# Kernel tuning notes

Measured on AMD Instinct MI355X. Metric: run time of the kernel, lower is better.

## Reference

```python
import jax, jax.numpy as jnp
import numpy as np

GRID_SIZE = 8
POSITIVE_MARGIN = 1.0
NEGATIVE_MARGIN = 0.2
LAMBDA_D = 250.0
B, Hc, Wc, D = 4, 60, 60, 64


def warp_points(points, homographies):
    """points: [N,2] in (y,x); homographies: [B,3,3]. Returns [B,N,2] in (y,x)."""
    n = points.shape[0]
    xy1 = jnp.concatenate([points[:, ::-1], jnp.ones((n, 1), points.dtype)], axis=-1)  # (x,y,1)
    w = jnp.einsum('bij,nj->bni', homographies, xy1)  # [B,N,3]
    w = w[..., :2] / w[..., 2:3]
    return w[..., ::-1]  # back to (y,x)


def setup_inputs() -> dict:
    key = jax.random.key(0)
    k1, k2, k3 = jax.random.split(key, 3)
    descriptors = jax.random.normal(k1, (B, Hc, Wc, D), dtype=jnp.float32)
    warped_descriptors = jax.random.normal(k2, (B, Hc, Wc, D), dtype=jnp.float32)
    # near-identity homographies so warped cell centers remain close to the grid
    homographies = jnp.eye(3, dtype=jnp.float32)[None] + 0.001 * jax.random.normal(
        k3, (B, 3, 3), dtype=jnp.float32)
    valid_mask = jnp.ones((B, Hc * GRID_SIZE, Wc * GRID_SIZE), dtype=jnp.float32)
    return {"descriptors": descriptors, "warped_descriptors": warped_descriptors,
            "homographies": homographies, "valid_mask": valid_mask}


def reference(descriptors, warped_descriptors, homographies, valid_mask):
    b, hc, wc, d = descriptors.shape
    g = GRID_SIZE

    # cell-center coordinates (y, x) at full resolution
    yy, xx = jnp.meshgrid(jnp.arange(hc), jnp.arange(wc), indexing='ij')
    coord_cells = jnp.stack([yy, xx], axis=-1).astype(jnp.float32) * g + g // 2  # [Hc,Wc,2]

    warped_coord_cells = warp_points(coord_cells.reshape(-1, 2), homographies)  # [B,Hc*Wc,2]
    cc = coord_cells.reshape(1, 1, 1, hc, wc, 2)
    wcc = warped_coord_cells.reshape(b, hc, wc, 1, 1, 2)
    cell_distances = jnp.linalg.norm(cc - wcc, axis=-1)  # [B,Hc,Wc,Hc,Wc]
    s = (cell_distances <= g - 0.5).astype(descriptors.dtype)

    # broadcast dot-product score tensor [B,Hc,Wc,Hc,Wc]
    dot = jnp.einsum('bijd,bkld->bijkl', descriptors, warped_descriptors)

    positive_dist = jnp.maximum(0.0, POSITIVE_MARGIN - dot)
    negative_dist = jnp.maximum(0.0, dot - NEGATIVE_MARGIN)
    loss = LAMBDA_D * s * positive_dist + (1.0 - s) * negative_dist

    # space-to-depth + prod over the g*g block == per-cell AND of the valid mask
    vm = valid_mask.reshape(b, hc, g, wc, g)
    vm = jnp.prod(vm, axis=(2, 4))  # [B,Hc,Wc]
    vm = vm.reshape(b, 1, 1, hc, wc)

    normalization = jnp.sum(vm) * jnp.float32(hc * wc)
    return jnp.sum(vm * loss) / normalization
```

## Files before the change

kernel.cpp:

```cpp
#include <hip/hip_runtime.h>
#include <hip/hip_bf16.h>
#include <hip/hip_fp8.h>

#define HC 60
#define WCC 60
#define DD 64
#define NCELL (HC * WCC)
#define NBC (4 * NCELL)
#define IMG (HC * 8)
#define MPAD 3840
#define NT2 30
#define GEMM_BLOCKS (NT2 * NT2 * 4)
#define CHUNK (GEMM_BLOCKS / 8)

#define CVT_BLOCKS 480
#define VM_BLOCKS 57
#define WC_BLOCKS 60
#define PREP_BLOCKS (CVT_BLOCKS + VM_BLOCKS + WC_BLOCKS)

typedef float f32x4 __attribute__((ext_vector_type(4)));
typedef unsigned long long u64x2 __attribute__((ext_vector_type(2)));

__device__ inline unsigned char f2fp8(float f) {
    __hip_fp8_e4m3 h(f);
    return h.__x;
}

__device__ inline void gload_lds16(const void* g, void* l) {
    __builtin_amdgcn_global_load_lds(
        (const __attribute__((address_space(1))) unsigned int*)g,
        (__attribute__((address_space(3))) unsigned int*)l, 16, 0, 0);
}

__device__ inline int div60(int v) { return (v * 17477) >> 20; }


__global__ __launch_bounds__(256) void dl_prep_kernel(
    const float* __restrict__ desc, const float* __restrict__ wdesc,
    const float* __restrict__ homog, const float* __restrict__ mask,
    unsigned char* __restrict__ descb, unsigned char* __restrict__ wdescb,
    float* __restrict__ vm, float* __restrict__ vpart, float2* __restrict__ wcent)
{
    const int bid = blockIdx.x;
    const int tid = threadIdx.x;

    if (bid < CVT_BLOCKS) {
        int k = bid & 7;
        int q = bid >> 3;
        int b = k >> 1;
        int wp = (k & 1) * 60 + q;
        int row = wp * 32 + (tid >> 3);
        int c = tid & 7;
        unsigned long long pa = 0ull, pb = 0ull;
        if (row < NCELL) {
            size_t src = ((size_t)(b * NCELL + row)) * DD + c * 8;
            float4 a0 = *(const float4*)(desc + src);
            float4 a1 = *(const float4*)(desc + src + 4);
            float4 b0 = *(const float4*)(wdesc + src);
            float4 b1 = *(const float4*)(wdesc + src + 4);
            pa = (unsigned long long)f2fp8(a0.x)
               | ((unsigned long long)f2fp8(a0.y) << 8)
               | ((unsigned long long)f2fp8(a0.z) << 16)
               | ((unsigned long long)f2fp8(a0.w) << 24)
               | ((unsigned long long)f2fp8(a1.x) << 32)
               | ((unsigned long long)f2fp8(a1.y) << 40)
               | ((unsigned long long)f2fp8(a1.z) << 48)
               | ((unsigned long long)f2fp8(a1.w) << 56);
            pb = (unsigned long long)f2fp8(b0.x)
               | ((unsigned long long)f2fp8(b0.y) << 8)
               | ((unsigned long long)f2fp8(b0.z) << 16)
               | ((unsigned long long)f2fp8(b0.w) << 24)
               | ((unsigned long long)f2fp8(b1.x) << 32)
               | ((unsigned long long)f2fp8(b1.y) << 40)
               | ((unsigned long long)f2fp8(b1.z) << 48)
               | ((unsigned long long)f2fp8(b1.w) << 56);
        }
        int pos = ((c & 3) * 16 + (c >> 2) * 8) ^ ((row & 3) << 4);
        size_t dst = ((size_t)b * MPAD + row) * 64 + pos;
        *(unsigned long long*)(descb + dst) = pa;
        *(unsigned long long*)(wdescb + dst) = pb;
    } else if (bid < CVT_BLOCKS + VM_BLOCKS) {
        int vb = bid - CVT_BLOCKS;
        int cell = vb * 256 + tid;
        float v = 0.f;
        if (cell < NBC) {
            int b = cell / NCELL;
            int rem = cell % NCELL;
            int k = rem / WCC, l = rem % WCC;
            const float* p = mask + (size_t)b * IMG * IMG + (size_t)(k * 8) * IMG + l * 8;
            float prod = 1.f;
#pragma unroll
            for (int dy = 0; dy < 8; ++dy) {
                float4 a0 = *(const float4*)(p + (size_t)dy * IMG);
                float4 a1 = *(const float4*)(p + (size_t)dy * IMG + 4);
                prod *= a0.x * a0.y * a0.z * a0.w * a1.x * a1.y * a1.z * a1.w;
            }
            vm[cell] = prod;
            v = prod;
        }
#pragma unroll
        for (int off = 32; off > 0; off >>= 1) v += __shfl_xor(v, off);
        __shared__ float sp[4];
        if ((tid & 63) == 0) sp[tid >> 6] = v;
        __syncthreads();
        if (tid == 0) vpart[vb] = sp[0] + sp[1] + sp[2] + sp[3];
    } else {
        int t = (bid - CVT_BLOCKS - VM_BLOCKS) * 256 + tid;
        int b = t / MPAD;
        int r = t - b * MPAD;
        float2 o;
        if (r < NCELL) {
            int i = div60(r);
            int j = r - i * WCC;
            const float* H = homog + b * 9;
            float x = (float)(j * 8 + 4), y = (float)(i * 8 + 4);
            float X2 = H[6] * x + H[7] * y + H[8];
            o.x = (H[3] * x + H[4] * y + H[5]) / X2;
            o.y = (H[0] * x + H[1] * y + H[2]) / X2;
        } else {
            o.x = 1e9f; o.y = 1e9f;
        }
        wcent[t] = o;
    }
}

__global__ __launch_bounds__(256, 3) void dl_gemm_loss_kernel(
    const unsigned char* __restrict__ descb, const unsigned char* __restrict__ wdescb,
    const float* __restrict__ vm, const float2* __restrict__ wcent,
    float* __restrict__ gpart)
{
    __shared__ unsigned char sA[128 * 64];
    __shared__ unsigned char sB[128 * 64];
    __shared__ float2 swc[128];
    __shared__ float swave[4];

    const int orig = blockIdx.x;
    const int tile = (orig & 7) * CHUNK + (orig >> 3);
    const int b = tile / (NT2 * NT2);
    const int rr = tile - b * (NT2 * NT2);
    const int x = rr / NT2;
    const int y = rr - x * NT2;
    const int m0 = x * 128;
    const int n0 = y * 128;

    const int tid = threadIdx.x;
    const int lane = tid & 63;
    const int wv = tid >> 6;

    const unsigned char* gA = descb + ((size_t)b * MPAD + m0) * 64;
    const unsigned char* gB = wdescb + ((size_t)b * MPAD + n0) * 64;

#pragma unroll
    for (int t = 0; t < 2; ++t) {
        gload_lds16(gA + t * 4096 + tid * 16, sA + t * 4096 + tid * 16);
        gload_lds16(gB + t * 4096 + tid * 16, sB + t * 4096 + tid * 16);
    }
    if (tid < 128) swc[tid] = wcent[b * MPAD + m0 + tid];

    const int wr = wv >> 1, wcs = wv & 1;
    const int frow = lane & 15;
    const int kg16 = (lane >> 4) * 16;

    float cyv[4], cxv[4], vmv[4];
#pragma unroll
    for (int fj = 0; fj < 4; ++fj) {
        int col = n0 + wcs * 64 + fj * 16 + frow;
        int k = div60(col);
        int l = col - k * WCC;
        cyv[fj] = (float)(k * 8 + 4);
        cxv[fj] = (float)(l * 8 + 4);
        vmv[fj] = (col < NCELL) ? vm[b * NCELL + col] : 0.f;
    }
    float wyl = wcent[b * MPAD + m0 + wr * 64 + lane].x;
    float wlo = wyl, whi = wyl;
#pragma unroll
    for (int off = 32; off > 0; off >>= 1) {
        wlo = fminf(wlo, __shfl_xor(wlo, off));
        whi = fmaxf(whi, __shfl_xor(whi, off));
    }
    int c0 = n0 + wcs * 64;
    float cy0 = (float)(div60(c0) * 8 + 4) - 7.5f;
    float cy1 = (float)(div60(c0 + 63) * 8 + 4) + 7.5f;
    bool full = (whi >= cy0) && (wlo <= cy1);

    __syncthreads();

    u64x2 afr[4], bfr[4];
#pragma unroll
    for (int f = 0; f < 4; ++f) {
        int ra = wr * 64 + f * 16 + frow;
        afr[f] = *(const u64x2*)(sA + ra * 64 + (kg16 ^ ((ra & 3) << 4)));
        int rb = wcs * 64 + f * 16 + frow;
        bfr[f] = *(const u64x2*)(sB + rb * 64 + (kg16 ^ ((rb & 3) << 4)));
    }

    f32x4 acc[4][4];
#pragma unroll
    for (int i2 = 0; i2 < 4; ++i2)
#pragma unroll
        for (int j2 = 0; j2 < 4; ++j2)
            acc[i2][j2] = (f32x4)(0.f);

#pragma unroll
    for (int kk = 0; kk < 2; ++kk)
#pragma unroll
        for (int fi = 0; fi < 4; ++fi)
#pragma unroll
            for (int fj = 0; fj < 4; ++fj)
                acc[fi][fj] = __builtin_amdgcn_mfma_f32_16x16x32_fp8_fp8(
                    (long long)afr[fi][kk], (long long)bfr[fj][kk],
                    acc[fi][fj], 0, 0, 0);

    float partial = 0.f;
    if (full) {
#pragma unroll
        for (int fi = 0; fi < 4; ++fi) {
#pragma unroll
            for (int q = 0; q < 4; ++q) {
                float2 w2 = swc[wr * 64 + fi * 16 + (lane >> 4) * 4 + q];
#pragma unroll
                for (int fj = 0; fj < 4; ++fj) {
                    float dot = acc[fi][fj][q];
                    float ddy = cyv[fj] - w2.x;
                    float ddx = cxv[fj] - w2.y;
                    float d2 = ddy * ddy + ddx * ddx;
                    float pos = 250.f * fmaxf(1.f - dot, 0.f) + 0.2f;
                    float neg = fmaxf(dot, 0.2f);
                    partial += vmv[fj] * ((d2 <= 56.25f) ? pos : neg);
                }
            }
        }
    } else {
#pragma unroll
        for (int fj = 0; fj < 4; ++fj) {
            float cs = 0.f;
#pragma unroll
            for (int fi = 0; fi < 4; ++fi)
#pragma unroll
                for (int q = 0; q < 4; ++q)
                    cs += fmaxf(acc[fi][fj][q], 0.2f);
            partial = fmaf(vmv[fj], cs, partial);
        }
    }

#pragma unroll
    for (int off = 32; off > 0; off >>= 1) partial += __shfl_xor(partial, off);
    if (lane == 0) swave[wv] = partial;
    __syncthreads();
    if (tid == 0)
        gpart[orig] = swave[0] + swave[1] + swave[2] + swave[3];
}

__global__ __launch_bounds__(256) void dl_final_kernel(
    const float* __restrict__ vpart, const float* __restrict__ gpart,
    float* __restrict__ out)
{
    int tid = threadIdx.x;
    float ls = 0.f, vs = 0.f;
    for (int i = tid; i < GEMM_BLOCKS; i += 256) ls += gpart[i];
    for (int i = tid; i < VM_BLOCKS; i += 256) vs += vpart[i];
#pragma unroll
    for (int off = 32; off > 0; off >>= 1) {
        ls += __shfl_xor(ls, off);
        vs += __shfl_xor(vs, off);
    }
    __shared__ float sl[4], sv[4];
    if ((tid & 63) == 0) { sl[tid >> 6] = ls; sv[tid >> 6] = vs; }
    __syncthreads();
    if (tid == 0) {
        float L = sl[0] + sl[1] + sl[2] + sl[3];
        float V = sv[0] + sv[1] + sv[2] + sv[3];
        L -= 0.2f * (float)MPAD * V;
        out[0] = L / (V * (float)NCELL);
    }
}

extern "C" void kernel_launch(void* const* d_in, const int* in_sizes, int n_in,
                              void* d_out, int out_size, void* d_ws, size_t ws_size,
                              hipStream_t stream) {
    const float* desc  = (const float*)d_in[0];
    const float* wdesc = (const float*)d_in[1];
    const float* homog = (const float*)d_in[2];
    const float* mask  = (const float*)d_in[3];
    float* out = (float*)d_out;
    float* wsf = (float*)d_ws;

    float* vpart = wsf;
    float* vm    = wsf + 64;
    float* gpart = wsf + 64 + NBC;
    float2* wcent = (float2*)(wsf + 18064);
    unsigned char* descb  = (unsigned char*)(wsf + 48896);
    unsigned char* wdescb = descb + (size_t)4 * MPAD * 64;

    hipLaunchKernelGGL(dl_prep_kernel, dim3(PREP_BLOCKS), dim3(256), 0, stream,
                       desc, wdesc, homog, mask, descb, wdescb, vm, vpart, wcent);
    hipLaunchKernelGGL(dl_gemm_loss_kernel, dim3(GEMM_BLOCKS), dim3(256), 0, stream,
                       descb, wdescb, vm, wcent, gpart);
    hipLaunchKernelGGL(dl_final_kernel, dim3(1), dim3(256), 0, stream,
                       vpart, gpart, out);
}
```

Baseline: 31.60 us.

## Make GEMM tile loads wave-private and drop block-level barriers

Each wave now loads its own 64-row slices of A and B into private LDS buffers and waits with s_waitcnt vmcnt(0) instead of a block __syncthreads. The shared warped-center LDS buffer is dropped in favour of direct global reads. Each wave writes its own partial sum, which removes the final barrier and LDS reduction; the final kernel sums four times as many partials. In exchange, A and B slices are loaded twice per block and LDS use doubles, which may lower occupancy.

```diff
diff --git a/kernel.cpp b/kernel.cpp
--- a/kernel.cpp
+++ b/kernel.cpp
@@ -12,6 +12,7 @@
 #define NT2 30
 #define GEMM_BLOCKS (NT2 * NT2 * 4)
 #define CHUNK (GEMM_BLOCKS / 8)
+#define GPARTS (GEMM_BLOCKS * 4)
 
 #define CVT_BLOCKS 480
 #define VM_BLOCKS 57
@@ -129,10 +130,8 @@
     const float* __restrict__ vm, const float2* __restrict__ wcent,
     float* __restrict__ gpart)
 {
-    __shared__ unsigned char sA[128 * 64];
-    __shared__ unsigned char sB[128 * 64];
-    __shared__ float2 swc[128];
-    __shared__ float swave[4];
+    __shared__ unsigned char sA[4][4096];
+    __shared__ unsigned char sB[4][4096];
 
     const int orig = blockIdx.x;
     const int tile = (orig & 7) * CHUNK + (orig >> 3);
@@ -146,18 +145,18 @@
     const int tid = threadIdx.x;
     const int lane = tid & 63;
     const int wv = tid >> 6;
-
-    const unsigned char* gA = descb + ((size_t)b * MPAD + m0) * 64;
-    const unsigned char* gB = wdescb + ((size_t)b * MPAD + n0) * 64;
-
-#pragma unroll
-    for (int t = 0; t < 2; ++t) {
-        gload_lds16(gA + t * 4096 + tid * 16, sA + t * 4096 + tid * 16);
-        gload_lds16(gB + t * 4096 + tid * 16, sB + t * 4096 + tid * 16);
-    }
-    if (tid < 128) swc[tid] = wcent[b * MPAD + m0 + tid];
-
     const int wr = wv >> 1, wcs = wv & 1;
+
+    {
+        const unsigned char* gA = descb + ((size_t)b * MPAD + m0 + wr * 64) * 64;
+        const unsigned char* gB = wdescb + ((size_t)b * MPAD + n0 + wcs * 64) * 64;
+#pragma unroll
+        for (int t = 0; t < 4; ++t) {
+            gload_lds16(gA + t * 1024 + lane * 16, sA[wv] + t * 1024 + lane * 16);
+            gload_lds16(gB + t * 1024 + lane * 16, sB[wv] + t * 1024 + lane * 16);
+        }
+    }
+
     const int frow = lane & 15;
     const int kg16 = (lane >> 4) * 16;
 
@@ -171,7 +170,8 @@
         cxv[fj] = (float)(l * 8 + 4);
         vmv[fj] = (col < NCELL) ? vm[b * NCELL + col] : 0.f;
     }
-    float wyl = wcent[b * MPAD + m0 + wr * 64 + lane].x;
+    const int rowbase = b * MPAD + m0 + wr * 64;
+    float wyl = wcent[rowbase + lane].x;
     float wlo = wyl, whi = wyl;
 #pragma unroll
     for (int off = 32; off > 0; off >>= 1) {
@@ -183,15 +183,14 @@
     float cy1 = (float)(div60(c0 + 63) * 8 + 4) + 7.5f;
     bool full = (whi >= cy0) && (wlo <= cy1);
 
-    __syncthreads();
+    asm volatile("s_waitcnt vmcnt(0)" ::: "memory");
 
     u64x2 afr[4], bfr[4];
 #pragma unroll
     for (int f = 0; f < 4; ++f) {
-        int ra = wr * 64 + f * 16 + frow;
-        afr[f] = *(const u64x2*)(sA + ra * 64 + (kg16 ^ ((ra & 3) << 4)));
-        int rb = wcs * 64 + f * 16 + frow;
-        bfr[f] = *(const u64x2*)(sB + rb * 64 + (kg16 ^ ((rb & 3) << 4)));
+        int ra = f * 16 + frow;
+        afr[f] = *(const u64x2*)(sA[wv] + ra * 64 + (kg16 ^ ((ra & 3) << 4)));
+        bfr[f] = *(const u64x2*)(sB[wv] + ra * 64 + (kg16 ^ ((ra & 3) << 4)));
     }
 
     f32x4 acc[4][4];
@@ -217,7 +216,7 @@
         for (int fi = 0; fi < 4; ++fi) {
 #pragma unroll
             for (int q = 0; q < 4; ++q) {
-                float2 w2 = swc[wr * 64 + fi * 16 + (lane >> 4) * 4 + q];
+                float2 w2 = wcent[rowbase + fi * 16 + (lane >> 4) * 4 + q];
 #pragma unroll
                 for (int fj = 0; fj < 4; ++fj) {
                     float dot = acc[fi][fj][q];
@@ -245,10 +244,7 @@
 
 #pragma unroll
     for (int off = 32; off > 0; off >>= 1) partial += __shfl_xor(partial, off);
-    if (lane == 0) swave[wv] = partial;
-    __syncthreads();
-    if (tid == 0)
-        gpart[orig] = swave[0] + swave[1] + swave[2] + swave[3];
+    if (lane == 0) gpart[orig * 4 + wv] = partial;
 }
 
 __global__ __launch_bounds__(256) void dl_final_kernel(
@@ -257,7 +253,7 @@
 {
     int tid = threadIdx.x;
     float ls = 0.f, vs = 0.f;
-    for (int i = tid; i < GEMM_BLOCKS; i += 256) ls += gpart[i];
+    for (int i = tid; i < GPARTS; i += 256) ls += gpart[i];
     for (int i = tid; i < VM_BLOCKS; i += 256) vs += vpart[i];
 #pragma unroll
     for (int off = 32; off > 0; off >>= 1) {
@@ -287,9 +283,9 @@
 
     float* vpart = wsf;
     float* vm    = wsf + 64;
-    float* gpart = wsf + 64 + NBC;
-    float2* wcent = (float2*)(wsf + 18064);
-    unsigned char* descb  = (unsigned char*)(wsf + 48896);
+    float* gpart = wsf + 14464;
+    float2* wcent = (float2*)(wsf + 28864);
+    unsigned char* descb  = (unsigned char*)(wsf + 59648);
     unsigned char* wdescb = descb + (size_t)4 * MPAD * 64;
 
     hipLaunchKernelGGL(dl_prep_kernel, dim3(PREP_BLOCKS), dim3(256), 0, stream,
```

Result: slower. 42.12 us (+33.3%).
